# Optimization experiments

Measured on AMD Instinct MI355X. Metric: run time of the kernel, lower is better.

Reference implementation:

```python
import jax, jax.numpy as jnp
import numpy as np

N, E = 50000, 800000
IN, HID, PROJ = 256, 256, 256


def setup_inputs() -> dict:
    key = jax.random.key(0)
    ks = jax.random.split(key, 6)
    x = jax.random.normal(ks[0], (N, IN), dtype=jnp.float32)
    edge_index = jax.random.randint(ks[1], (2, E), 0, N, dtype=jnp.int32)
    # GCNConv params: Linear (no bias inside lin; bias added after aggregation)
    W1 = jax.random.normal(ks[2], (IN, HID), dtype=jnp.float32) / np.sqrt(IN)
    b1 = jnp.zeros((HID,), dtype=jnp.float32)
    W2 = jax.random.normal(ks[3], (HID, PROJ), dtype=jnp.float32) / np.sqrt(HID)
    b2 = jnp.zeros((PROJ,), dtype=jnp.float32)
    # shared PReLU parameter (PyTorch default init 0.25, single shared scalar)
    a = jnp.asarray(0.25, dtype=jnp.float32)
    return {"x": x, "W1": W1, "b1": b1, "W2": W2, "b2": b2, "a": a,
            "edge_index": edge_index}


def _prelu(x, a):
    return jnp.where(x >= 0, x, a * x)


def _gcn_conv(x, W, b, src, dst, norm):
    # GCNConv: out = D^-1/2 (A + I) D^-1/2 (x W) + b
    h = x @ W                                      # [N, out]
    msg = h[src] * norm[:, None]                   # [E+N, out] edge messages
    out = jax.ops.segment_sum(msg, dst, num_segments=N)
    return out + b


def reference(x, W1, b1, W2, b2, a, edge_index):
    src, dst = edge_index[0], edge_index[1]
    loop = jnp.arange(N, dtype=src.dtype)
    src = jnp.concatenate([src, loop])             # add self-loops
    dst = jnp.concatenate([dst, loop])
    # symmetric normalization (degree counted on dst, as in PyG gcn_norm)
    deg = jax.ops.segment_sum(jnp.ones_like(dst, jnp.float32), dst,
                              num_segments=N)
    dinv = jax.lax.rsqrt(jnp.maximum(deg, 1.0))    # deg >= 1 with self-loops
    norm = dinv[src] * dinv[dst]                   # [E+N]
    h = _prelu(_gcn_conv(x, W1, b1, src, dst, norm), a)
    h = _prelu(_gcn_conv(h, W2, b2, src, dst, norm), a)
    return h
```

## Files before the change

kernel.cpp:

```cpp
#include <hip/hip_runtime.h>

#define NN 50000
#define EE 800000
#define FF 256
#define NBLK 196

typedef float    f32x4 __attribute__((ext_vector_type(4)));
typedef _Float16 f16x8 __attribute__((ext_vector_type(8)));
typedef _Float16 f16x4 __attribute__((ext_vector_type(4)));


__global__ void count_kernel(const int* __restrict__ ei, int* __restrict__ ec) {
    int e = blockIdx.x * 256 + threadIdx.x;
    if (e < EE) atomicAdd(&ec[ei[EE + e]], 1);
}

__global__ __launch_bounds__(256) void scan_part(const int* __restrict__ ec,
                                                 int* __restrict__ bsum) {
    int i = blockIdx.x * 256 + threadIdx.x;
    int v = (i < NN) ? ec[i] : 0;
#pragma unroll
    for (int d = 1; d < 64; d <<= 1) v += __shfl_xor(v, d);
    __shared__ int wt[4];
    int lane = threadIdx.x & 63, wid = threadIdx.x >> 6;
    if (lane == 0) wt[wid] = v;
    __syncthreads();
    if (threadIdx.x == 0)
        bsum[blockIdx.x] = wt[0] + wt[1] + wt[2] + wt[3];
}

__global__ __launch_bounds__(256) void scan_mid(const int* __restrict__ bsum,
                                                int* __restrict__ boff,
                                                int* __restrict__ rs) {
    const int t = threadIdx.x;
    int v = (t < NBLK) ? bsum[t] : 0;
    int lane = t & 63, wid = t >> 6;
    int x = v;
#pragma unroll
    for (int d = 1; d < 64; d <<= 1) {
        int u = __shfl_up(x, d);
        if (lane >= d) x += u;
    }
    __shared__ int wt[4];
    if (lane == 63) wt[wid] = x;
    __syncthreads();
    int add = 0;
    for (int wi = 0; wi < wid; ++wi) add += wt[wi];
    x += add;
    if (t < NBLK) boff[t] = x - v;
    if (t == NBLK - 1) rs[NN] = x;
}

__global__ __launch_bounds__(256) void scan_final(const int* __restrict__ ec,
                                                  const int* __restrict__ boff,
                                                  int* __restrict__ rs,
                                                  float* __restrict__ dinv) {
    int i = blockIdx.x * 256 + threadIdx.x;
    int v = (i < NN) ? ec[i] : 0;
    int lane = threadIdx.x & 63, wid = threadIdx.x >> 6;
    int x = v;
#pragma unroll
    for (int d = 1; d < 64; d <<= 1) {
        int u = __shfl_up(x, d);
        if (lane >= d) x += u;
    }
    __shared__ int wt[4];
    if (lane == 63) wt[wid] = x;
    __syncthreads();
    int add = 0;
    for (int wi = 0; wi < wid; ++wi) add += wt[wi];
    x += add;
    if (i < NN) {
        rs[i]   = x - v + boff[blockIdx.x];
        dinv[i] = rsqrtf((float)(v + 1));
    }
}

__global__ void fill_kernel(const int* __restrict__ ei, const int* __restrict__ rs,
                            int* __restrict__ cnt, const float* __restrict__ dinv,
                            int2* __restrict__ ecw) {
    int e = blockIdx.x * 256 + threadIdx.x;
    if (e >= EE) return;
    int s = ei[e];
    int d = ei[EE + e];
    int p = rs[d] + atomicAdd(&cnt[d], 1);
    ecw[p] = make_int2(s, __float_as_int(dinv[s]));
}

__global__ void packw_kernel(const float* __restrict__ W1, const float* __restrict__ W2,
                             _Float16* __restrict__ wp) {
    int idx = blockIdx.x * 256 + threadIdx.x;
    int p   = idx & 511;
    int kt  = (idx >> 9) & 7;
    int nb  = (idx >> 12) & 1;
    int L   = (idx >> 13) & 1;
    const float* W = L ? W2 : W1;
    int rs = p >> 2, cs = p & 3;
    int r  = rs ^ ((rs >> 2) & 1);
    int c  = cs ^ (r & 3);
    int n  = nb * 128 + r;
    int k0 = kt * 32 + c * 8;
    f16x8 hi, lo;
#pragma unroll
    for (int j = 0; j < 8; ++j) {
        float v = W[(size_t)(k0 + j) * 256 + n];
        _Float16 h = (_Float16)v;
        hi[j] = h;
        lo[j] = (_Float16)(v - (float)h);
    }
    size_t ch = ((size_t)((L * 2 + 0) * 2 + nb) * 8 + kt) * 4096;
    size_t cl = ((size_t)((L * 2 + 1) * 2 + nb) * 8 + kt) * 4096;
    *(f16x8*)(wp + ch + (size_t)p * 8) = hi;
    *(f16x8*)(wp + cl + (size_t)p * 8) = lo;
}


__device__ __forceinline__ void gll16(const void* g, void* l) {
    __builtin_amdgcn_global_load_lds(
        (const __attribute__((address_space(1))) void*)g,
        (__attribute__((address_space(3))) void*)l, 16, 0, 0);
}

template<typename AT>
__global__ __launch_bounds__(512) void gemm_kernel(
    const AT* __restrict__ X, const _Float16* __restrict__ Bhi,
    const _Float16* __restrict__ Blo, _Float16* __restrict__ H) {
    __shared__ __align__(16) _Float16 Bh[2][4096];
    __shared__ __align__(16) _Float16 Bl[2][4096];
    __shared__ __align__(16) AT       As[2][4096];

    const int tid = threadIdx.x;
    const int ln  = tid & 63;
    const int w   = tid >> 6;
    const int wm  = w & 1;
    const int wn  = w >> 1;
    const int q   = ln >> 4;
    const int l16 = ln & 15;
    const int m0  = blockIdx.y * 128;
    const int nb  = blockIdx.x;
    const size_t bchunk = (size_t)nb * 8 * 4096;

    f32x4 acc[4][2] = {};

    auto stage = [&](int kt, int buf) {
        int g = w * 64 + ln;
        gll16(Bhi + bchunk + (size_t)kt * 4096 + (size_t)g * 8,
              &Bh[buf][w * 512]);
        gll16(Blo + bchunk + (size_t)kt * 4096 + (size_t)g * 8,
              &Bl[buf][w * 512]);
        if constexpr (sizeof(AT) == 4) {
#pragma unroll
            for (int p = 0; p < 2; ++p) {
                int gg = p * 512 + w * 64 + ln;
                int rs = gg >> 3, cs = gg & 7;
                int c  = cs ^ (rs & 7);
                int gm = m0 + rs; if (gm > NN - 1) gm = NN - 1;
                gll16((const float*)X + (size_t)gm * FF + kt * 32 + c * 4,
                      (float*)&As[buf][0] + (size_t)(p * 512 + w * 64) * 4);
            }
        } else {
            int rs = g >> 2, cs = g & 3;
            int r  = rs ^ ((rs >> 2) & 1);
            int c  = cs ^ (r & 3);
            int gm = m0 + r; if (gm > NN - 1) gm = NN - 1;
            gll16((const _Float16*)X + (size_t)gm * FF + kt * 32 + c * 8,
                  (_Float16*)&As[buf][0] + (size_t)(w * 64) * 8);
        }
    };

    auto compute = [&](int buf) {
        f16x8 af[4], bhf[2], blf[2];
#pragma unroll
        for (int mt = 0; mt < 4; ++mt) {
            int r = wm * 64 + mt * 16 + l16;
            if constexpr (sizeof(AT) == 4) {
                const float* Ab = (const float*)&As[buf][0];
                f32x4 v0 = *(const f32x4*)(Ab + (size_t)(r * 8 + ((2 * q)     ^ (r & 7))) * 4);
                f32x4 v1 = *(const f32x4*)(Ab + (size_t)(r * 8 + ((2 * q + 1) ^ (r & 7))) * 4);
                f16x8 a;
                a[0] = (_Float16)v0.x; a[1] = (_Float16)v0.y;
                a[2] = (_Float16)v0.z; a[3] = (_Float16)v0.w;
                a[4] = (_Float16)v1.x; a[5] = (_Float16)v1.y;
                a[6] = (_Float16)v1.z; a[7] = (_Float16)v1.w;
                af[mt] = a;
            } else {
                const _Float16* Ab = (const _Float16*)&As[buf][0];
                int rr = r ^ ((r >> 2) & 1);
                af[mt] = *(const f16x8*)(Ab + (size_t)(rr * 4 + (q ^ (r & 3))) * 8);
            }
        }
#pragma unroll
        for (int nt = 0; nt < 2; ++nt) {
            int r  = wn * 32 + nt * 16 + l16;
            int rr = r ^ ((r >> 2) & 1);
            int off = (rr * 4 + (q ^ (r & 3))) * 8;
            bhf[nt] = *(const f16x8*)(&Bh[buf][off]);
            blf[nt] = *(const f16x8*)(&Bl[buf][off]);
        }
#pragma unroll
        for (int mt = 0; mt < 4; ++mt)
#pragma unroll
            for (int nt = 0; nt < 2; ++nt) {
                acc[mt][nt] = __builtin_amdgcn_mfma_f32_16x16x32_f16(af[mt], bhf[nt], acc[mt][nt], 0, 0, 0);
                acc[mt][nt] = __builtin_amdgcn_mfma_f32_16x16x32_f16(af[mt], blf[nt], acc[mt][nt], 0, 0, 0);
            }
    };

    stage(0, 0);
    __syncthreads();
    int cur = 0;
#pragma unroll
    for (int kt = 0; kt < 8; ++kt) {
        if (kt < 7) stage(kt + 1, cur ^ 1);
        compute(cur);
        __syncthreads();
        cur ^= 1;
    }

#pragma unroll
    for (int mt = 0; mt < 4; ++mt)
#pragma unroll
        for (int r4 = 0; r4 < 4; ++r4) {
            int m = m0 + wm * 64 + mt * 16 + q * 4 + r4;
            if (m < NN) {
#pragma unroll
                for (int nt = 0; nt < 2; ++nt) {
                    int n = nb * 128 + wn * 32 + nt * 16 + l16;
                    H[(size_t)m * FF + n] = (_Float16)acc[mt][nt][r4];
                }
            }
        }
}

template<typename OT>
__global__ __launch_bounds__(256) void agg_kernel(
    const _Float16* __restrict__ H, const int* __restrict__ rs,
    const int2* __restrict__ ecw, const float* __restrict__ dinv,
    const float* __restrict__ bias, const float* __restrict__ a_ptr,
    OT* __restrict__ out) {
    const int row  = blockIdx.x * 4 + (threadIdx.x >> 6);
    const int lane = threadIdx.x & 63;
    if (row >= NN) return;

    const float av = a_ptr[0];
    const float di = dinv[row];

    f16x4 hv = *(const f16x4*)(H + (size_t)row * FF + lane * 4);
    float ax = di * (float)hv.x;
    float ay = di * (float)hv.y;
    float az = di * (float)hv.z;
    float aw = di * (float)hv.w;

    int e   = rs[row];
    int end = rs[row + 1];
    for (; e + 3 < end; e += 4) {
        int2 p0 = ecw[e], p1 = ecw[e + 1], p2 = ecw[e + 2], p3 = ecw[e + 3];
        f16x4 h0 = *(const f16x4*)(H + (size_t)p0.x * FF + lane * 4);
        f16x4 h1 = *(const f16x4*)(H + (size_t)p1.x * FF + lane * 4);
        f16x4 h2 = *(const f16x4*)(H + (size_t)p2.x * FF + lane * 4);
        f16x4 h3 = *(const f16x4*)(H + (size_t)p3.x * FF + lane * 4);
        float w0 = __int_as_float(p0.y), w1 = __int_as_float(p1.y);
        float w2 = __int_as_float(p2.y), w3 = __int_as_float(p3.y);
        ax += w0 * (float)h0.x + w1 * (float)h1.x + w2 * (float)h2.x + w3 * (float)h3.x;
        ay += w0 * (float)h0.y + w1 * (float)h1.y + w2 * (float)h2.y + w3 * (float)h3.y;
        az += w0 * (float)h0.z + w1 * (float)h1.z + w2 * (float)h2.z + w3 * (float)h3.z;
        aw += w0 * (float)h0.w + w1 * (float)h1.w + w2 * (float)h2.w + w3 * (float)h3.w;
    }
    for (; e < end; ++e) {
        int2 p = ecw[e];
        float w0 = __int_as_float(p.y);
        f16x4 h0 = *(const f16x4*)(H + (size_t)p.x * FF + lane * 4);
        ax += w0 * (float)h0.x;
        ay += w0 * (float)h0.y;
        az += w0 * (float)h0.z;
        aw += w0 * (float)h0.w;
    }

    f32x4 bv = *(const f32x4*)(bias + lane * 4);
    float r0 = di * ax + bv.x; r0 = (r0 >= 0.f) ? r0 : av * r0;
    float r1 = di * ay + bv.y; r1 = (r1 >= 0.f) ? r1 : av * r1;
    float r2 = di * az + bv.z; r2 = (r2 >= 0.f) ? r2 : av * r2;
    float r3 = di * aw + bv.w; r3 = (r3 >= 0.f) ? r3 : av * r3;
    if constexpr (sizeof(OT) == 4) {
        f32x4 res = {r0, r1, r2, r3};
        *(f32x4*)((float*)out + (size_t)row * FF + lane * 4) = res;
    } else {
        f16x4 res;
        res.x = (_Float16)r0; res.y = (_Float16)r1;
        res.z = (_Float16)r2; res.w = (_Float16)r3;
        *(f16x4*)((_Float16*)out + (size_t)row * FF + lane * 4) = res;
    }
}

extern "C" void kernel_launch(void* const* d_in, const int* in_sizes, int n_in,
                              void* d_out, int out_size, void* d_ws, size_t ws_size,
                              hipStream_t stream) {
    const float* x  = (const float*)d_in[0];
    const float* W1 = (const float*)d_in[1];
    const float* b1 = (const float*)d_in[2];
    const float* W2 = (const float*)d_in[3];
    const float* b2 = (const float*)d_in[4];
    const float* a  = (const float*)d_in[5];
    const int*   ei = (const int*)d_in[6];
    float* out = (float*)d_out;

    char* ws = (char*)d_ws;
    size_t off = 0;
    auto carve = [&](size_t bytes) -> char* {
        char* p = ws + off;
        off = (off + bytes + 255) & ~(size_t)255;
        return p;
    };
    int*      ec   = (int*)carve((size_t)NN * 4);
    int*      cnt  = (int*)carve((size_t)NN * 4);
    int*      rs   = (int*)carve((size_t)(NN + 1) * 4);
    float*    dinv = (float*)carve((size_t)NN * 4);
    int*      bsum = (int*)carve((size_t)NBLK * 4);
    int*      boff = (int*)carve((size_t)NBLK * 4);
    int2*     ecw  = (int2*)carve((size_t)EE * 8);
    _Float16* wp   = (_Float16*)carve((size_t)4 * 65536 * 2);
    _Float16* h    = (_Float16*)carve((size_t)NN * FF * 2);
    _Float16* h1   = (_Float16*)carve((size_t)NN * FF * 2);

    hipMemsetAsync(ec, 0, (size_t)NN * 4, stream);
    hipMemsetAsync(cnt, 0, (size_t)NN * 4, stream);

    count_kernel<<<(EE + 255) / 256, 256, 0, stream>>>(ei, ec);
    scan_part <<<NBLK, 256, 0, stream>>>(ec, bsum);
    scan_mid  <<<1, 256, 0, stream>>>(bsum, boff, rs);
    scan_final<<<NBLK, 256, 0, stream>>>(ec, boff, rs, dinv);
    fill_kernel<<<(EE + 255) / 256, 256, 0, stream>>>(ei, rs, cnt, dinv, ecw);
    packw_kernel<<<64, 256, 0, stream>>>(W1, W2, wp);

    gemm_kernel<float><<<dim3(2, 391), 512, 0, stream>>>(
        x, wp, wp + 65536, h);
    agg_kernel<_Float16><<<(NN + 3) / 4, 256, 0, stream>>>(h, rs, ecw, dinv, b1, a, h1);
    gemm_kernel<_Float16><<<dim3(2, 391), 512, 0, stream>>>(
        h1, wp + 131072, wp + 131072 + 65536, h);
    agg_kernel<float><<<(NN + 3) / 4, 256, 0, stream>>>(h, rs, ecw, dinv, b2, a, out);
}
```

Before: 361.4 us.

## Slice aggregation by feature column and swizzle GEMM block order

The aggregation kernel now splits each row's 256 features into 8 slices of 32 handled by separate blocks. Within a wavefront, 8 groups process different edges in parallel and are combined with a cross-lane shuffle reduction. Edge records are read with nontemporal loads and prefetched one ahead. The GEMM uses a 1D grid remapped so that both N-halves of neighbouring M-tiles run close together, aiming to improve L2 reuse of A rows. The aggregation change trades launching 8x more blocks, and re-reading the edge list once per slice, for shorter per-lane edge chains and better cache locality of the gathered feature slices.

```diff
diff --git a/kernel.cpp b/kernel.cpp
--- a/kernel.cpp
+++ b/kernel.cpp
@@ -129,6 +129,11 @@
     __shared__ __align__(16) _Float16 Bl[2][4096];
     __shared__ __align__(16) AT       As[2][4096];
 
+    const int gid = blockIdx.x;
+    const int p_  = (gid >> 4) * 8 + (gid & 7);
+    const int nb  = (gid >> 3) & 1;
+    if (p_ >= 391) return;
+
     const int tid = threadIdx.x;
     const int ln  = tid & 63;
     const int w   = tid >> 6;
@@ -136,8 +141,7 @@
     const int wn  = w >> 1;
     const int q   = ln >> 4;
     const int l16 = ln & 15;
-    const int m0  = blockIdx.y * 128;
-    const int nb  = blockIdx.x;
+    const int m0  = p_ * 128;
     const size_t bchunk = (size_t)nb * 8 * 4096;
 
     f32x4 acc[4][2] = {};
@@ -150,17 +154,17 @@
               &Bl[buf][w * 512]);
         if constexpr (sizeof(AT) == 4) {
 #pragma unroll
-            for (int p = 0; p < 2; ++p) {
-                int gg = p * 512 + w * 64 + ln;
-                int rs = gg >> 3, cs = gg & 7;
-                int c  = cs ^ (rs & 7);
-                int gm = m0 + rs; if (gm > NN - 1) gm = NN - 1;
+            for (int pp = 0; pp < 2; ++pp) {
+                int gg = pp * 512 + w * 64 + ln;
+                int rss = gg >> 3, cs = gg & 7;
+                int c  = cs ^ (rss & 7);
+                int gm = m0 + rss; if (gm > NN - 1) gm = NN - 1;
                 gll16((const float*)X + (size_t)gm * FF + kt * 32 + c * 4,
-                      (float*)&As[buf][0] + (size_t)(p * 512 + w * 64) * 4);
+                      (float*)&As[buf][0] + (size_t)(pp * 512 + w * 64) * 4);
             }
         } else {
-            int rs = g >> 2, cs = g & 3;
-            int r  = rs ^ ((rs >> 2) & 1);
+            int rss = g >> 2, cs = g & 3;
+            int r  = rss ^ ((rss >> 2) & 1);
             int c  = cs ^ (r & 3);
             int gm = m0 + r; if (gm > NN - 1) gm = NN - 1;
             gll16((const _Float16*)X + (size_t)gm * FF + kt * 32 + c * 8,
@@ -238,57 +242,68 @@
     const int2* __restrict__ ecw, const float* __restrict__ dinv,
     const float* __restrict__ bias, const float* __restrict__ a_ptr,
     OT* __restrict__ out) {
-    const int row  = blockIdx.x * 4 + (threadIdx.x >> 6);
+    const int slice = blockIdx.x & 7;
+    const int row   = (blockIdx.x >> 3) * 4 + (threadIdx.x >> 6);
+    if (row >= NN) return;
     const int lane = threadIdx.x & 63;
-    if (row >= NN) return;
+    const int g    = lane >> 3;
+    const int t    = lane & 7;
+    const int f0   = slice * 32 + t * 4;
 
     const float av = a_ptr[0];
     const float di = dinv[row];
 
-    f16x4 hv = *(const f16x4*)(H + (size_t)row * FF + lane * 4);
-    float ax = di * (float)hv.x;
-    float ay = di * (float)hv.y;
-    float az = di * (float)hv.z;
-    float aw = di * (float)hv.w;
-
-    int e   = rs[row];
-    int end = rs[row + 1];
-    for (; e + 3 < end; e += 4) {
-        int2 p0 = ecw[e], p1 = ecw[e + 1], p2 = ecw[e + 2], p3 = ecw[e + 3];
-        f16x4 h0 = *(const f16x4*)(H + (size_t)p0.x * FF + lane * 4);
-        f16x4 h1 = *(const f16x4*)(H + (size_t)p1.x * FF + lane * 4);
-        f16x4 h2 = *(const f16x4*)(H + (size_t)p2.x * FF + lane * 4);
-        f16x4 h3 = *(const f16x4*)(H + (size_t)p3.x * FF + lane * 4);
-        float w0 = __int_as_float(p0.y), w1 = __int_as_float(p1.y);
-        float w2 = __int_as_float(p2.y), w3 = __int_as_float(p3.y);
-        ax += w0 * (float)h0.x + w1 * (float)h1.x + w2 * (float)h2.x + w3 * (float)h3.x;
-        ay += w0 * (float)h0.y + w1 * (float)h1.y + w2 * (float)h2.y + w3 * (float)h3.y;
-        az += w0 * (float)h0.z + w1 * (float)h1.z + w2 * (float)h2.z + w3 * (float)h3.z;
-        aw += w0 * (float)h0.w + w1 * (float)h1.w + w2 * (float)h2.w + w3 * (float)h3.w;
-    }
-    for (; e < end; ++e) {
-        int2 p = ecw[e];
-        float w0 = __int_as_float(p.y);
-        f16x4 h0 = *(const f16x4*)(H + (size_t)p.x * FF + lane * 4);
-        ax += w0 * (float)h0.x;
-        ay += w0 * (float)h0.y;
-        az += w0 * (float)h0.z;
-        aw += w0 * (float)h0.w;
-    }
-
-    f32x4 bv = *(const f32x4*)(bias + lane * 4);
-    float r0 = di * ax + bv.x; r0 = (r0 >= 0.f) ? r0 : av * r0;
-    float r1 = di * ay + bv.y; r1 = (r1 >= 0.f) ? r1 : av * r1;
-    float r2 = di * az + bv.z; r2 = (r2 >= 0.f) ? r2 : av * r2;
-    float r3 = di * aw + bv.w; r3 = (r3 >= 0.f) ? r3 : av * r3;
-    if constexpr (sizeof(OT) == 4) {
-        f32x4 res = {r0, r1, r2, r3};
-        *(f32x4*)((float*)out + (size_t)row * FF + lane * 4) = res;
-    } else {
-        f16x4 res;
-        res.x = (_Float16)r0; res.y = (_Float16)r1;
-        res.z = (_Float16)r2; res.w = (_Float16)r3;
-        *(f16x4*)((_Float16*)out + (size_t)row * FF + lane * 4) = res;
+    float ax = 0.f, ay = 0.f, az = 0.f, aw = 0.f;
+    if (g == 0) {
+        f16x4 hv = *(const f16x4*)(H + (size_t)row * FF + f0);
+        ax = di * (float)hv.x; ay = di * (float)hv.y;
+        az = di * (float)hv.z; aw = di * (float)hv.w;
+    }
+
+    int e = rs[row] + g;
+    const int end = rs[row + 1];
+    if (e < end) {
+        long long pv = __builtin_nontemporal_load((const long long*)(ecw + e));
+        while (true) {
+            e += 8;
+            const bool more = (e < end);
+            long long pn = 0;
+            if (more) pn = __builtin_nontemporal_load((const long long*)(ecw + e));
+            int   src = (int)(unsigned)(pv & 0xffffffffLL);
+            float w0  = __int_as_float((int)(pv >> 32));
+            f16x4 h0  = *(const f16x4*)(H + (size_t)src * FF + f0);
+            ax += w0 * (float)h0.x;
+            ay += w0 * (float)h0.y;
+            az += w0 * (float)h0.z;
+            aw += w0 * (float)h0.w;
+            if (!more) break;
+            pv = pn;
+        }
+    }
+
+#pragma unroll
+    for (int d = 8; d < 64; d <<= 1) {
+        ax += __shfl_xor(ax, d);
+        ay += __shfl_xor(ay, d);
+        az += __shfl_xor(az, d);
+        aw += __shfl_xor(aw, d);
+    }
+
+    if (g == 0) {
+        f32x4 bv = *(const f32x4*)(bias + f0);
+        float r0 = di * ax + bv.x; r0 = (r0 >= 0.f) ? r0 : av * r0;
+        float r1 = di * ay + bv.y; r1 = (r1 >= 0.f) ? r1 : av * r1;
+        float r2 = di * az + bv.z; r2 = (r2 >= 0.f) ? r2 : av * r2;
+        float r3 = di * aw + bv.w; r3 = (r3 >= 0.f) ? r3 : av * r3;
+        if constexpr (sizeof(OT) == 4) {
+            f32x4 res = {r0, r1, r2, r3};
+            *(f32x4*)((float*)out + (size_t)row * FF + f0) = res;
+        } else {
+            f16x4 res;
+            res.x = (_Float16)r0; res.y = (_Float16)r1;
+            res.z = (_Float16)r2; res.w = (_Float16)r3;
+            *(f16x4*)((_Float16*)out + (size_t)row * FF + f0) = res;
+        }
     }
 }
 
@@ -332,10 +347,8 @@
     fill_kernel<<<(EE + 255) / 256, 256, 0, stream>>>(ei, rs, cnt, dinv, ecw);
     packw_kernel<<<64, 256, 0, stream>>>(W1, W2, wp);
 
-    gemm_kernel<float><<<dim3(2, 391), 512, 0, stream>>>(
-        x, wp, wp + 65536, h);
-    agg_kernel<_Float16><<<(NN + 3) / 4, 256, 0, stream>>>(h, rs, ecw, dinv, b1, a, h1);
-    gemm_kernel<_Float16><<<dim3(2, 391), 512, 0, stream>>>(
-        h1, wp + 131072, wp + 131072 + 65536, h);
-    agg_kernel<float><<<(NN + 3) / 4, 256, 0, stream>>>(h, rs, ecw, dinv, b2, a, out);
-}
+    gemm_kernel<float><<<784, 512, 0, stream>>>(x, wp, wp + 65536, h);
+    agg_kernel<_Float16><<<12500 * 8, 256, 0, stream>>>(h, rs, ecw, dinv, b1, a, h1);
+    gemm_kernel<_Float16><<<784, 512, 0, stream>>>(h1, wp + 131072, wp + 131072 + 65536, h);
+    agg_kernel<float><<<12500 * 8, 256, 0, stream>>>(h, rs, ecw, dinv, b2, a, out);
+}
```

Result: slower. 629.3 us (+74.1%).

## Fuse degree counting into first GEMM launch, swizzle GEMM grid, unroll aggregation by 8

Applied to the files above, without the earlier changes.

The edge-degree counting kernel is folded into the first GEMM launch as extra trailing blocks, so one launch is dropped and the atomics can run alongside the GEMM tiles. The GEMM now uses a 1D grid with a grouped swizzle, so pairs of column blocks for the same row tiles run close together and share X rows in cache. The aggregation loop gains an 8-way unrolled body that keeps more gather loads in flight. The risks are that the fused counting blocks carry the GEMM's large LDS footprint, and that the wider unroll raises register pressure.

```diff
diff --git a/kernel.cpp b/kernel.cpp
--- a/kernel.cpp
+++ b/kernel.cpp
@@ -4,16 +4,13 @@
 #define EE 800000
 #define FF 256
 #define NBLK 196
+#define GEMM_BLKS 784
+#define CNT_BLKS 1563
 
 typedef float    f32x4 __attribute__((ext_vector_type(4)));
 typedef _Float16 f16x8 __attribute__((ext_vector_type(8)));
 typedef _Float16 f16x4 __attribute__((ext_vector_type(4)));
 
-
-__global__ void count_kernel(const int* __restrict__ ei, int* __restrict__ ec) {
-    int e = blockIdx.x * 256 + threadIdx.x;
-    if (e < EE) atomicAdd(&ec[ei[EE + e]], 1);
-}
 
 __global__ __launch_bounds__(256) void scan_part(const int* __restrict__ ec,
                                                  int* __restrict__ bsum) {
@@ -124,10 +121,24 @@
 template<typename AT>
 __global__ __launch_bounds__(512) void gemm_kernel(
     const AT* __restrict__ X, const _Float16* __restrict__ Bhi,
-    const _Float16* __restrict__ Blo, _Float16* __restrict__ H) {
+    const _Float16* __restrict__ Blo, _Float16* __restrict__ H,
+    const int* __restrict__ ei, int* __restrict__ ec) {
     __shared__ __align__(16) _Float16 Bh[2][4096];
     __shared__ __align__(16) _Float16 Bl[2][4096];
     __shared__ __align__(16) AT       As[2][4096];
+
+    if constexpr (sizeof(AT) == 4) {
+        if (blockIdx.x >= GEMM_BLKS) {
+            int e = (blockIdx.x - GEMM_BLKS) * 512 + threadIdx.x;
+            if (e < EE) atomicAdd(&ec[ei[EE + e]], 1);
+            return;
+        }
+    }
+
+    const int gid = blockIdx.x;
+    const int p_  = (gid >> 4) * 8 + (gid & 7);
+    const int nb  = (gid >> 3) & 1;
+    if (p_ >= 391) return;
 
     const int tid = threadIdx.x;
     const int ln  = tid & 63;
@@ -136,8 +147,7 @@
     const int wn  = w >> 1;
     const int q   = ln >> 4;
     const int l16 = ln & 15;
-    const int m0  = blockIdx.y * 128;
-    const int nb  = blockIdx.x;
+    const int m0  = p_ * 128;
     const size_t bchunk = (size_t)nb * 8 * 4096;
 
     f32x4 acc[4][2] = {};
@@ -150,17 +160,17 @@
               &Bl[buf][w * 512]);
         if constexpr (sizeof(AT) == 4) {
 #pragma unroll
-            for (int p = 0; p < 2; ++p) {
-                int gg = p * 512 + w * 64 + ln;
-                int rs = gg >> 3, cs = gg & 7;
-                int c  = cs ^ (rs & 7);
-                int gm = m0 + rs; if (gm > NN - 1) gm = NN - 1;
+            for (int pp = 0; pp < 2; ++pp) {
+                int gg = pp * 512 + w * 64 + ln;
+                int rss = gg >> 3, cs = gg & 7;
+                int c  = cs ^ (rss & 7);
+                int gm = m0 + rss; if (gm > NN - 1) gm = NN - 1;
                 gll16((const float*)X + (size_t)gm * FF + kt * 32 + c * 4,
-                      (float*)&As[buf][0] + (size_t)(p * 512 + w * 64) * 4);
+                      (float*)&As[buf][0] + (size_t)(pp * 512 + w * 64) * 4);
             }
         } else {
-            int rs = g >> 2, cs = g & 3;
-            int r  = rs ^ ((rs >> 2) & 1);
+            int rss = g >> 2, cs = g & 3;
+            int r  = rss ^ ((rss >> 2) & 1);
             int c  = cs ^ (r & 3);
             int gm = m0 + r; if (gm > NN - 1) gm = NN - 1;
             gll16((const _Float16*)X + (size_t)gm * FF + kt * 32 + c * 8,
@@ -253,6 +263,30 @@
 
     int e   = rs[row];
     int end = rs[row + 1];
+    for (; e + 7 < end; e += 8) {
+        int2 p0 = ecw[e],     p1 = ecw[e + 1], p2 = ecw[e + 2], p3 = ecw[e + 3];
+        int2 p4 = ecw[e + 4], p5 = ecw[e + 5], p6 = ecw[e + 6], p7 = ecw[e + 7];
+        f16x4 h0 = *(const f16x4*)(H + (size_t)p0.x * FF + lane * 4);
+        f16x4 h1 = *(const f16x4*)(H + (size_t)p1.x * FF + lane * 4);
+        f16x4 h2 = *(const f16x4*)(H + (size_t)p2.x * FF + lane * 4);
+        f16x4 h3 = *(const f16x4*)(H + (size_t)p3.x * FF + lane * 4);
+        f16x4 h4 = *(const f16x4*)(H + (size_t)p4.x * FF + lane * 4);
+        f16x4 h5 = *(const f16x4*)(H + (size_t)p5.x * FF + lane * 4);
+        f16x4 h6 = *(const f16x4*)(H + (size_t)p6.x * FF + lane * 4);
+        f16x4 h7 = *(const f16x4*)(H + (size_t)p7.x * FF + lane * 4);
+        float w0 = __int_as_float(p0.y), w1 = __int_as_float(p1.y);
+        float w2 = __int_as_float(p2.y), w3 = __int_as_float(p3.y);
+        float w4 = __int_as_float(p4.y), w5 = __int_as_float(p5.y);
+        float w6 = __int_as_float(p6.y), w7 = __int_as_float(p7.y);
+        ax += w0 * (float)h0.x + w1 * (float)h1.x + w2 * (float)h2.x + w3 * (float)h3.x
+            + w4 * (float)h4.x + w5 * (float)h5.x + w6 * (float)h6.x + w7 * (float)h7.x;
+        ay += w0 * (float)h0.y + w1 * (float)h1.y + w2 * (float)h2.y + w3 * (float)h3.y
+            + w4 * (float)h4.y + w5 * (float)h5.y + w6 * (float)h6.y + w7 * (float)h7.y;
+        az += w0 * (float)h0.z + w1 * (float)h1.z + w2 * (float)h2.z + w3 * (float)h3.z
+            + w4 * (float)h4.z + w5 * (float)h5.z + w6 * (float)h6.z + w7 * (float)h7.z;
+        aw += w0 * (float)h0.w + w1 * (float)h1.w + w2 * (float)h2.w + w3 * (float)h3.w
+            + w4 * (float)h4.w + w5 * (float)h5.w + w6 * (float)h6.w + w7 * (float)h7.w;
+    }
     for (; e + 3 < end; e += 4) {
         int2 p0 = ecw[e], p1 = ecw[e + 1], p2 = ecw[e + 2], p3 = ecw[e + 3];
         f16x4 h0 = *(const f16x4*)(H + (size_t)p0.x * FF + lane * 4);
@@ -325,17 +359,18 @@
     hipMemsetAsync(ec, 0, (size_t)NN * 4, stream);
     hipMemsetAsync(cnt, 0, (size_t)NN * 4, stream);
 
-    count_kernel<<<(EE + 255) / 256, 256, 0, stream>>>(ei, ec);
+    packw_kernel<<<64, 256, 0, stream>>>(W1, W2, wp);
+
+    gemm_kernel<float><<<GEMM_BLKS + CNT_BLKS, 512, 0, stream>>>(
+        x, wp, wp + 65536, h, ei, ec);
+
     scan_part <<<NBLK, 256, 0, stream>>>(ec, bsum);
     scan_mid  <<<1, 256, 0, stream>>>(bsum, boff, rs);
     scan_final<<<NBLK, 256, 0, stream>>>(ec, boff, rs, dinv);
     fill_kernel<<<(EE + 255) / 256, 256, 0, stream>>>(ei, rs, cnt, dinv, ecw);
-    packw_kernel<<<64, 256, 0, stream>>>(W1, W2, wp);
-
-    gemm_kernel<float><<<dim3(2, 391), 512, 0, stream>>>(
-        x, wp, wp + 65536, h);
+
     agg_kernel<_Float16><<<(NN + 3) / 4, 256, 0, stream>>>(h, rs, ecw, dinv, b1, a, h1);
-    gemm_kernel<_Float16><<<dim3(2, 391), 512, 0, stream>>>(
-        h1, wp + 131072, wp + 131072 + 65536, h);
+    gemm_kernel<_Float16><<<GEMM_BLKS, 512, 0, stream>>>(
+        h1, wp + 131072, wp + 131072 + 65536, h, nullptr, nullptr);
     agg_kernel<float><<<(NN + 3) / 4, 256, 0, stream>>>(h, rs, ecw, dinv, b2, a, out);
 }
```

After: 342.9 us. -5.1%, faster.
